# Kernel optimization log

Hardware: AMD Instinct MI355X
Metric: run time of the kernel (lower is better)

## Reference

```python
import jax, jax.numpy as jnp
import numpy as np
import math

D = 256        # embedding_size
NHEAD = 4
HD = D // NHEAD
FF = 2048      # torch TransformerEncoderLayer default dim_feedforward
NLAYER = 3
VOCAB = 30000
OLD = 2048     # resnet50 fc in_features
BPTT = 20
EOS = 2
PAD = 0
MAXLEN = 5000


def make_pe():
    position = np.arange(MAXLEN)[:, None].astype(np.float32)
    div_term = np.exp(np.arange(0, D, 2).astype(np.float32) * (-math.log(10000.0) / D))
    pe = np.zeros((MAXLEN, D), dtype=np.float32)
    pe[:, 0::2] = np.sin(position * div_term)
    pe[:, 1::2] = np.cos(position * div_term)
    return jnp.asarray(pe)  # [maxlen, d]

PE = make_pe()


def setup_inputs() -> dict:
    key = jax.random.key(0)
    ks = jax.random.split(key, 20)
    s = 0.02
    inp = {
        'image_feats': jax.random.normal(ks[0], (64, OLD), jnp.float32),
        'target_ingrs': jax.random.randint(ks[1], (64, BPTT), 0, VOCAB),
        'emb_table': jax.random.normal(ks[2], (VOCAB, D), jnp.float32) * s,
        'W_g2e': jax.random.normal(ks[3], (OLD, D), jnp.float32) * s,
        'b_g2e': jnp.zeros((D,), jnp.float32),
        'W_out': jax.random.normal(ks[4], (D, VOCAB), jnp.float32) * s,
        'b_out': jnp.zeros((VOCAB,), jnp.float32),
    }
    # per-layer transformer params
    Wqkv, bqkv, Wo, bo, W1, b1, W2, b2, g1, be1, g2, be2 = ([] for _ in range(12))
    k = ks[5]
    for l in range(NLAYER):
        k, *sub = jax.random.split(k, 7)
        Wqkv.append(jax.random.normal(sub[0], (D, 3 * D), jnp.float32) * s)
        bqkv.append(jnp.zeros((3 * D,), jnp.float32))
        Wo.append(jax.random.normal(sub[1], (D, D), jnp.float32) * s)
        bo.append(jnp.zeros((D,), jnp.float32))
        W1.append(jax.random.normal(sub[2], (D, FF), jnp.float32) * s)
        b1.append(jnp.zeros((FF,), jnp.float32))
        W2.append(jax.random.normal(sub[3], (FF, D), jnp.float32) * s)
        b2.append(jnp.zeros((D,), jnp.float32))
        g1.append(jnp.ones((D,), jnp.float32)); be1.append(jnp.zeros((D,), jnp.float32))
        g2.append(jnp.ones((D,), jnp.float32)); be2.append(jnp.zeros((D,), jnp.float32))
    stk = lambda xs: jnp.stack(xs)
    inp.update(Wqkv=stk(Wqkv), bqkv=stk(bqkv), Wo=stk(Wo), bo=stk(bo),
               W1=stk(W1), b1=stk(b1), W2=stk(W2), b2=stk(b2),
               g1=stk(g1), be1=stk(be1), g2=stk(g2), be2=stk(be2))
    return inp


def layernorm(x, g, b):
    mu = jnp.mean(x, -1, keepdims=True)
    var = jnp.var(x, -1, keepdims=True)
    return (x - mu) * jax.lax.rsqrt(var + 1e-5) * g + b


def encoder(x, params):
    # x: [S, B, D] (seq-first like torch). Post-norm encoder, ReLU FFN, no mask.
    (Wqkv, bqkv, Wo, bo, W1, b1, W2, b2, g1, be1, g2, be2) = params
    S, B, _ = x.shape
    for l in range(NLAYER):
        qkv = x @ Wqkv[l] + bqkv[l]                  # [S,B,3D]
        q, k, v = jnp.split(qkv, 3, axis=-1)
        def heads(t):  # [S,B,D] -> [B,H,S,hd]
            return t.reshape(S, B, NHEAD, HD).transpose(1, 2, 0, 3)
        q, k, v = heads(q), heads(k), heads(v)
        att = jnp.einsum('bhqd,bhkd->bhqk', q, k) / math.sqrt(HD)
        att = jax.nn.softmax(att, axis=-1)
        o = jnp.einsum('bhqk,bhkd->bhqd', att, v)    # [B,H,S,hd]
        o = o.transpose(2, 0, 1, 3).reshape(S, B, D)
        x = layernorm(x + o @ Wo[l] + bo[l], g1[l], be1[l])
        ff = jax.nn.relu(x @ W1[l] + b1[l]) @ W2[l] + b2[l]
        x = layernorm(x + ff, g2[l], be2[l])
    return x


def mask_from_eos_after(ids):
    # mult_before=False: mask[:,idx] = all(ids[:,1:idx+1] != EOS); mask[:,0]=1
    ne = (ids != EOS)
    ne = ne.at[:, 0].set(True)
    return jnp.cumprod(ne.astype(jnp.int32), axis=1)  # [B,S]


def reference(image_feats, target_ingrs, emb_table, W_g2e, b_g2e, W_out, b_out,
              Wqkv, bqkv, Wo, bo, W1, b1, W2, b2, g1, be1, g2, be2):
    params = (Wqkv, bqkv, Wo, bo, W1, b1, W2, b2, g1, be1, g2, be2)
    B = image_feats.shape[0]
    img_embed = image_feats @ W_g2e + b_g2e          # [B,D]
    bptt = target_ingrs.shape[1]

    # embeds buffer: [bptt, B, D]; position 0 = image embed (note: original code
    # never applies pos_encoder in predict(), so neither do we)
    embeds = jnp.zeros((bptt, B, D), jnp.float32).at[0].set(img_embed)

    probs_steps = []
    words_steps = []
    # loop over decode steps (fixed-length Python loop; each step re-encodes prefix,
    # faithful to original no-KV-cache behavior)
    for i in range(bptt):
        seq = embeds[: i + 1]                        # [i+1, B, D]
        out = encoder(seq, params)[-1]               # [B, D]
        logits = out @ W_out + b_out                 # [B, V]
        sm = jax.nn.softmax(logits, axis=-1)
        widx = jnp.argmax(sm, axis=-1)               # [B]
        probs_steps.append(sm)
        words_steps.append(widx)
        if i + 1 < bptt:
            embeds = embeds.at[i + 1].set(emb_table[widx])

    decoder_out = jnp.stack(probs_steps, axis=1)     # [B, bptt, V]
    sampled_word = jnp.stack(words_steps, axis=1)    # [B, bptt]
    eos = decoder_out[:, :, EOS]
    mask = mask_from_eos_after(target_ingrs)         # [B, bptt] int
    ingr_probs = jnp.max(decoder_out * mask[:, :, None].astype(jnp.float32), axis=1)
    sampled_word = jnp.where(mask == 0, PAD, sampled_word)
    return ingr_probs, sampled_word, eos
```

## Files before the change

### kernel.cpp

```cpp
#include <hip/hip_runtime.h>
#include <math.h>

#define D 256
#define NH 4
#define HDIM 64
#define FFD 2048
#define NL 3
#define VOC 30000
#define BPTT 20
#define BATCH 64
#define NMAX (BPTT*BATCH)

__global__ void k_mask(const int* __restrict__ ids, int* __restrict__ mask) {
  int b = threadIdx.x;
  int run = 1;
  for (int j = 0; j < BPTT; ++j) {
    if (j > 0 && ids[b*BPTT + j] == 2) run = 0;
    mask[b*BPTT + j] = run;
  }
}

__global__ __launch_bounds__(256) void k_img(const float* __restrict__ feats,
                                             const float* __restrict__ Wg,
                                             const float* __restrict__ bg,
                                             float* __restrict__ embeds) {
  __shared__ float xs[2048];
  int b = blockIdx.x, tid = threadIdx.x;
  for (int j = 0; j < 8; ++j) xs[tid + j*256] = feats[b*2048 + tid + j*256];
  __syncthreads();
  float acc = 0.f;
  for (int k = 0; k < 2048; k += 4) {
    float4 xv = *(const float4*)&xs[k];
    acc += xv.x * Wg[(k+0)*D + tid];
    acc += xv.y * Wg[(k+1)*D + tid];
    acc += xv.z * Wg[(k+2)*D + tid];
    acc += xv.w * Wg[(k+3)*D + tid];
  }
  embeds[b*D + tid] = acc + bg[tid];
}

__global__ __launch_bounds__(256) void k_gemm8(
    const float* __restrict__ A, int lda,
    const float* __restrict__ W,
    const float* __restrict__ bias,
    float* __restrict__ C, long pstride,
    int klen, int M, int relu)
{
  __shared__ float As[8][256];
  const int tid  = threadIdx.x;
  const int tok0 = blockIdx.x * 8;
  const int colb = blockIdx.y * 256;
  const int z    = blockIdx.z;
  const int kbeg = z * klen;
  C += (long)z * pstride;
  const int colg = tid & 63;
  const int tokg = tid >> 6;
  const int col  = colb + colg*4;
  int colL = col;
  if (colL > M-4) colL = M-4;

  float acc[2][4] = {{0.f,0.f,0.f,0.f},{0.f,0.f,0.f,0.f}};

  for (int k0 = 0; k0 < klen; k0 += 256) {
    __syncthreads();
#pragma unroll
    for (int j = 0; j < 8; ++j)
      As[j][tid] = A[(long)(tok0 + j)*lda + kbeg + k0 + tid];
    __syncthreads();
    const float* Wp = W + (long)(kbeg + k0)*M + colL;
#pragma unroll 2
    for (int kk = 0; kk < 256; kk += 4) {
      float a[2][4], w[4][4];
      *(float4*)a[0] = *(const float4*)&As[tokg*2+0][kk];
      *(float4*)a[1] = *(const float4*)&As[tokg*2+1][kk];
      *(float4*)w[0] = *(const float4*)(Wp + (long)(kk+0)*M);
      *(float4*)w[1] = *(const float4*)(Wp + (long)(kk+1)*M);
      *(float4*)w[2] = *(const float4*)(Wp + (long)(kk+2)*M);
      *(float4*)w[3] = *(const float4*)(Wp + (long)(kk+3)*M);
#pragma unroll
      for (int j = 0; j < 2; ++j)
#pragma unroll
        for (int c = 0; c < 4; ++c)
#pragma unroll
          for (int q = 0; q < 4; ++q)
            acc[j][c] += a[j][q] * w[q][c];
    }
  }

  if (col < M) {
    float bv[4] = {0.f,0.f,0.f,0.f};
    if (bias) *(float4*)bv = *(const float4*)(bias + col);
#pragma unroll
    for (int j = 0; j < 2; ++j) {
      float v[4];
#pragma unroll
      for (int c = 0; c < 4; ++c) {
        v[c] = acc[j][c] + bv[c];
        if (relu) v[c] = fmaxf(v[c], 0.f);
      }
      *(float4*)(C + (long)(tok0 + tokg*2 + j)*M + col) = *(float4*)v;
    }
  }
}

__global__ __launch_bounds__(256) void k_resln(
    const float* __restrict__ x, const float* __restrict__ parts, int nparts, long pstride,
    const float* __restrict__ bias, const float* __restrict__ g, const float* __restrict__ be,
    float* __restrict__ out)
{
  __shared__ float red[4];
  int tok = blockIdx.x, tid = threadIdx.x;
  float v = x[(long)tok*D + tid] + bias[tid];
  for (int p = 0; p < nparts; ++p) v += parts[(long)p*pstride + (long)tok*D + tid];

  float s = v;
  for (int off = 32; off; off >>= 1) s += __shfl_down(s, off);
  if ((tid & 63) == 0) red[tid >> 6] = s;
  __syncthreads();
  float mu = (red[0]+red[1]+red[2]+red[3]) * (1.0f/D);
  __syncthreads();
  float dv = v - mu;
  float q = dv*dv;
  for (int off = 32; off; off >>= 1) q += __shfl_down(q, off);
  if ((tid & 63) == 0) red[tid >> 6] = q;
  __syncthreads();
  float var = (red[0]+red[1]+red[2]+red[3]) * (1.0f/D);
  float inv = 1.0f / sqrtf(var + 1e-5f);
  out[(long)tok*D + tid] = dv * inv * g[tid] + be[tid];
}

__global__ __launch_bounds__(64) void k_attn(const float* __restrict__ qkv,
                                             float* __restrict__ o, int S)
{
  __shared__ float qs[BPTT*HDIM], ks[BPTT*HDIM], vs[BPTT*HDIM], ps[BPTT*(BPTT+1)];
  int bh = blockIdx.x;
  int b = bh & 63, h = bh >> 6;
  int d = threadIdx.x;
  for (int s = 0; s < S; ++s) {
    long base = (long)(s*BATCH + b)*(3*D) + h*HDIM + d;
    qs[s*HDIM+d] = qkv[base];
    ks[s*HDIM+d] = qkv[base + D];
    vs[s*HDIM+d] = qkv[base + 2*D];
  }
  __syncthreads();
  for (int p = d; p < S*S; p += 64) {
    int si = p / S, ti = p - si*S;
    float acc = 0.f;
#pragma unroll 4
    for (int k = 0; k < HDIM; ++k) acc += qs[si*HDIM+k] * ks[ti*HDIM+k];
    ps[si*(BPTT+1)+ti] = acc * 0.125f;
  }
  __syncthreads();
  if (d < S) {
    float m = -1e30f;
    for (int t = 0; t < S; ++t) m = fmaxf(m, ps[d*(BPTT+1)+t]);
    float sum = 0.f;
    for (int t = 0; t < S; ++t) { float e = expf(ps[d*(BPTT+1)+t] - m); ps[d*(BPTT+1)+t] = e; sum += e; }
    float inv = 1.0f / sum;
    for (int t = 0; t < S; ++t) ps[d*(BPTT+1)+t] *= inv;
  }
  __syncthreads();
  for (int s = 0; s < S; ++s) {
    float acc = 0.f;
    for (int t = 0; t < S; ++t) acc += ps[s*(BPTT+1)+t] * vs[t*HDIM+d];
    o[(long)(s*BATCH+b)*D + h*HDIM + d] = acc;
  }
}

__global__ __launch_bounds__(256) void k_vocab(
    const float* __restrict__ logits, const int* __restrict__ mask,
    float* __restrict__ out_probs, float* __restrict__ out_words, float* __restrict__ out_eos,
    const float* __restrict__ emb, float* __restrict__ embeds, int step)
{
  __shared__ float redA[4];
  __shared__ float r_s[4];
  __shared__ float r_em[4];
  __shared__ int   r_ei[4];
  int b = blockIdx.x, tid = threadIdx.x;
  const float* lrow = logits + (long)b*VOC;

  float m = -1e30f;
  for (int c = tid; c < VOC; c += 256) m = fmaxf(m, lrow[c]);
  for (int off = 32; off; off >>= 1) m = fmaxf(m, __shfl_down(m, off));
  if ((tid & 63) == 0) redA[tid >> 6] = m;
  __syncthreads();
  float gmax = fmaxf(fmaxf(redA[0],redA[1]), fmaxf(redA[2],redA[3]));
  __syncthreads();

  float s = 0.f, em = -1.0f;
  int ei = VOC;
  for (int c = tid; c < VOC; c += 256) {
    float e = expf(lrow[c] - gmax);
    s += e;
    if (e > em) { em = e; ei = c; }
  }
  for (int off = 32; off; off >>= 1) {
    float em2 = __shfl_down(em, off);
    int   ei2 = __shfl_down(ei, off);
    if (em2 > em || (em2 == em && ei2 < ei)) { em = em2; ei = ei2; }
    s += __shfl_down(s, off);
  }
  if ((tid & 63) == 0) { r_s[tid>>6] = s; r_em[tid>>6] = em; r_ei[tid>>6] = ei; }
  __syncthreads();
  float Ssum = r_s[0]+r_s[1]+r_s[2]+r_s[3];
  em = r_em[0]; ei = r_ei[0];
  for (int w = 1; w < 4; ++w)
    if (r_em[w] > em || (r_em[w] == em && r_ei[w] < ei)) { em = r_em[w]; ei = r_ei[w]; }

  int mk = mask[b*BPTT + step];

  for (int c = tid; c < VOC; c += 256) {
    float p = expf(lrow[c] - gmax) / Ssum;
    float* op = out_probs + (long)b*VOC + c;
    if (step == 0) *op = p;
    else if (mk)   *op = fmaxf(*op, p);
    if (c == 2) out_eos[b*BPTT + step] = p;
  }
  if (tid == 0) out_words[b*BPTT + step] = mk ? (float)ei : 0.0f;
  if (step + 1 < BPTT)
    embeds[(long)((step+1)*BATCH + b)*D + tid] = emb[(long)ei*D + tid];
}

extern "C" void kernel_launch(void* const* d_in, const int* in_sizes, int n_in,
                              void* d_out, int out_size, void* d_ws, size_t ws_size,
                              hipStream_t stream) {
  const float* image_feats = (const float*)d_in[0];
  const int*   target      = (const int*)  d_in[1];
  const float* emb_table   = (const float*)d_in[2];
  const float* W_g2e       = (const float*)d_in[3];
  const float* b_g2e       = (const float*)d_in[4];
  const float* W_out       = (const float*)d_in[5];
  const float* b_out       = (const float*)d_in[6];
  const float* Wqkv        = (const float*)d_in[7];
  const float* bqkv        = (const float*)d_in[8];
  const float* Wo          = (const float*)d_in[9];
  const float* bo          = (const float*)d_in[10];
  const float* W1          = (const float*)d_in[11];
  const float* b1          = (const float*)d_in[12];
  const float* W2          = (const float*)d_in[13];
  const float* b2          = (const float*)d_in[14];
  const float* g1          = (const float*)d_in[15];
  const float* be1         = (const float*)d_in[16];
  const float* g2          = (const float*)d_in[17];
  const float* be2         = (const float*)d_in[18];

  float* out_probs = (float*)d_out;
  float* out_words = out_probs + (long)BATCH*VOC;
  float* out_eos   = out_words + BATCH*BPTT;

  char* ws = (char*)d_ws;
  float* embeds = (float*)ws;  ws += sizeof(float)*(long)NMAX*D;
  float* xbuf   = (float*)ws;  ws += sizeof(float)*(long)NMAX*D;
  float* qkvb   = (float*)ws;  ws += sizeof(float)*(long)NMAX*3*D;
  float* obuf   = (float*)ws;  ws += sizeof(float)*(long)NMAX*D;
  float* pbuf   = (float*)ws;  ws += sizeof(float)*(long)4*NMAX*D;
  float* ffb    = (float*)ws;  ws += sizeof(float)*(long)NMAX*FFD;
  float* logits = (float*)ws;  ws += sizeof(float)*(long)BATCH*VOC;
  int*   maskb  = (int*)ws;    ws += sizeof(int)*BATCH*BPTT;

  k_mask<<<1, 64, 0, stream>>>(target, maskb);
  k_img<<<64, 256, 0, stream>>>(image_feats, W_g2e, b_g2e, embeds);

  for (int i = 0; i < BPTT; ++i) {
    int N = (i+1)*BATCH;
    for (int l = 0; l < NL; ++l) {
      const float* X = (l == 0) ? embeds : xbuf;
      k_gemm8<<<dim3(N/8, 3, 1), 256, 0, stream>>>(X, D, Wqkv + (long)l*D*3*D, bqkv + (long)l*3*D,
                                                   qkvb, 0, D, 3*D, 0);
      k_attn<<<dim3(BATCH*NH), 64, 0, stream>>>(qkvb, obuf, i+1);
      k_gemm8<<<dim3(N/8, 1, 1), 256, 0, stream>>>(obuf, D, Wo + (long)l*D*D, nullptr,
                                                   pbuf, 0, D, D, 0);
      k_resln<<<dim3(N), 256, 0, stream>>>(X, pbuf, 1, 0, bo + (long)l*D, g1 + (long)l*D, be1 + (long)l*D, xbuf);
      k_gemm8<<<dim3(N/8, FFD/256, 1), 256, 0, stream>>>(xbuf, D, W1 + (long)l*D*FFD, b1 + (long)l*FFD,
                                                         ffb, 0, D, FFD, 1);
      k_gemm8<<<dim3(N/8, 1, 4), 256, 0, stream>>>(ffb, FFD, W2 + (long)l*FFD*D, nullptr,
                                                   pbuf, (long)NMAX*D, FFD/4, D, 0);
      k_resln<<<dim3(N), 256, 0, stream>>>(xbuf, pbuf, 4, (long)NMAX*D, b2 + (long)l*D, g2 + (long)l*D, be2 + (long)l*D, xbuf);
    }
    k_gemm8<<<dim3(BATCH/8, (VOC+255)/256, 1), 256, 0, stream>>>(xbuf + (long)i*BATCH*D, D, W_out, b_out,
                                                                 logits, 0, D, VOC, 0);
    k_vocab<<<dim3(BATCH), 256, 0, stream>>>(logits, maskb, out_probs, out_words, out_eos,
                                             emb_table, embeds, i);
  }
}
```

Baseline: 10.87 ms.

## Replace per-op kernel launches with a single cooperative persistent megakernel

Fuses all stages of the decode loop into one cooperative kernel that uses grid-wide syncs between phases, so the roughly 700 separate launches disappear. It also fuses the Wo GEMM with the first residual+LayerNorm, fuses the FF1 GEMM with ReLU and a partial FF2 GEMM so the FF activation buffer is never written out, and gives attention four wavefronts per block. The cost is grid.sync overhead at each phase, a grid size hardcoded to 256 CUs, and load imbalance on the small early steps.

```diff
diff --git a/kernel.cpp b/kernel.cpp
--- a/kernel.cpp
+++ b/kernel.cpp
@@ -1,5 +1,8 @@
 #include <hip/hip_runtime.h>
+#include <hip/hip_cooperative_groups.h>
 #include <math.h>
+
+namespace cg = cooperative_groups;
 
 #define D 256
 #define NH 4
@@ -11,275 +14,380 @@
 #define BATCH 64
 #define NMAX (BPTT*BATCH)
 
-__global__ void k_mask(const int* __restrict__ ids, int* __restrict__ mask) {
-  int b = threadIdx.x;
-  int run = 1;
-  for (int j = 0; j < BPTT; ++j) {
-    if (j > 0 && ids[b*BPTT + j] == 2) run = 0;
-    mask[b*BPTT + j] = run;
+struct Params {
+  const float* image_feats;
+  const int*   target;
+  const float* emb_table;
+  const float* W_g2e;
+  const float* b_g2e;
+  const float* W_out;
+  const float* b_out;
+  const float* Wqkv; const float* bqkv;
+  const float* Wo;   const float* bo;
+  const float* W1;   const float* b1;
+  const float* W2;   const float* b2;
+  const float* g1;   const float* be1;
+  const float* g2;   const float* be2;
+  float* out_probs; float* out_words; float* out_eos;
+  float* embeds; float* xbuf; float* qkvb; float* obuf; float* pbuf; float* logits;
+  int* maskb;
+};
+
+union Smem {
+  struct { float As[8][256]; float ffs[8][256]; } g;
+  struct { float qs[BPTT*HDIM], ks[BPTT*HDIM], vs[BPTT*HDIM],
+                 ps[BPTT*(BPTT+1)]; } a;
+  struct { float red[4]; float r_s[4]; float r_em[4]; int r_ei[4]; } v;
+  float xs[2048];
+};
+
+__device__ __forceinline__ void tile_acc(const float (*As)[256], const float* __restrict__ Wp,
+                                         int M, int tokg, float acc[2][4]) {
+#pragma unroll 2
+  for (int kk = 0; kk < 256; kk += 4) {
+    float a0[4], a1[4], w[4][4];
+    *(float4*)a0 = *(const float4*)&As[tokg*2+0][kk];
+    *(float4*)a1 = *(const float4*)&As[tokg*2+1][kk];
+#pragma unroll
+    for (int q = 0; q < 4; ++q)
+      *(float4*)w[q] = *(const float4*)(Wp + (long)(kk+q)*M);
+#pragma unroll
+    for (int c = 0; c < 4; ++c)
+#pragma unroll
+      for (int q = 0; q < 4; ++q) {
+        acc[0][c] += a0[q]*w[q][c];
+        acc[1][c] += a1[q]*w[q][c];
+      }
   }
 }
 
-__global__ __launch_bounds__(256) void k_img(const float* __restrict__ feats,
-                                             const float* __restrict__ Wg,
-                                             const float* __restrict__ bg,
-                                             float* __restrict__ embeds) {
-  __shared__ float xs[2048];
-  int b = blockIdx.x, tid = threadIdx.x;
-  for (int j = 0; j < 8; ++j) xs[tid + j*256] = feats[b*2048 + tid + j*256];
-  __syncthreads();
-  float acc = 0.f;
-  for (int k = 0; k < 2048; k += 4) {
-    float4 xv = *(const float4*)&xs[k];
-    acc += xv.x * Wg[(k+0)*D + tid];
-    acc += xv.y * Wg[(k+1)*D + tid];
-    acc += xv.z * Wg[(k+2)*D + tid];
-    acc += xv.w * Wg[(k+3)*D + tid];
-  }
-  embeds[b*D + tid] = acc + bg[tid];
-}
-
-__global__ __launch_bounds__(256) void k_gemm8(
-    const float* __restrict__ A, int lda,
-    const float* __restrict__ W,
-    const float* __restrict__ bias,
-    float* __restrict__ C, long pstride,
-    int klen, int M, int relu)
-{
-  __shared__ float As[8][256];
-  const int tid  = threadIdx.x;
-  const int tok0 = blockIdx.x * 8;
-  const int colb = blockIdx.y * 256;
-  const int z    = blockIdx.z;
-  const int kbeg = z * klen;
-  C += (long)z * pstride;
-  const int colg = tid & 63;
-  const int tokg = tid >> 6;
-  const int col  = colb + colg*4;
-  int colL = col;
-  if (colL > M-4) colL = M-4;
-
-  float acc[2][4] = {{0.f,0.f,0.f,0.f},{0.f,0.f,0.f,0.f}};
-
-  for (int k0 = 0; k0 < klen; k0 += 256) {
+__global__ __launch_bounds__(256, 4) void mega(Params p) {
+  cg::grid_group grid = cg::this_grid();
+  const int wgid = blockIdx.x, nwg = gridDim.x, tid = threadIdx.x;
+  const int colg = tid & 63, tokg = tid >> 6;
+  __shared__ Smem sm;
+
+  if (wgid == 0 && tid < BATCH) {
+    int run = 1;
+    for (int j = 0; j < BPTT; ++j) {
+      if (j > 0 && p.target[tid*BPTT + j] == 2) run = 0;
+      p.maskb[tid*BPTT + j] = run;
+    }
+  }
+  for (int b = wgid; b < BATCH; b += nwg) {
     __syncthreads();
-#pragma unroll
-    for (int j = 0; j < 8; ++j)
-      As[j][tid] = A[(long)(tok0 + j)*lda + kbeg + k0 + tid];
+    for (int j = 0; j < 8; ++j) sm.xs[tid + j*256] = p.image_feats[b*2048 + tid + j*256];
     __syncthreads();
-    const float* Wp = W + (long)(kbeg + k0)*M + colL;
-#pragma unroll 2
-    for (int kk = 0; kk < 256; kk += 4) {
-      float a[2][4], w[4][4];
-      *(float4*)a[0] = *(const float4*)&As[tokg*2+0][kk];
-      *(float4*)a[1] = *(const float4*)&As[tokg*2+1][kk];
-      *(float4*)w[0] = *(const float4*)(Wp + (long)(kk+0)*M);
-      *(float4*)w[1] = *(const float4*)(Wp + (long)(kk+1)*M);
-      *(float4*)w[2] = *(const float4*)(Wp + (long)(kk+2)*M);
-      *(float4*)w[3] = *(const float4*)(Wp + (long)(kk+3)*M);
-#pragma unroll
-      for (int j = 0; j < 2; ++j)
-#pragma unroll
-        for (int c = 0; c < 4; ++c)
-#pragma unroll
-          for (int q = 0; q < 4; ++q)
-            acc[j][c] += a[j][q] * w[q][c];
-    }
-  }
-
-  if (col < M) {
-    float bv[4] = {0.f,0.f,0.f,0.f};
-    if (bias) *(float4*)bv = *(const float4*)(bias + col);
-#pragma unroll
-    for (int j = 0; j < 2; ++j) {
-      float v[4];
-#pragma unroll
-      for (int c = 0; c < 4; ++c) {
-        v[c] = acc[j][c] + bv[c];
-        if (relu) v[c] = fmaxf(v[c], 0.f);
-      }
-      *(float4*)(C + (long)(tok0 + tokg*2 + j)*M + col) = *(float4*)v;
-    }
-  }
-}
-
-__global__ __launch_bounds__(256) void k_resln(
-    const float* __restrict__ x, const float* __restrict__ parts, int nparts, long pstride,
-    const float* __restrict__ bias, const float* __restrict__ g, const float* __restrict__ be,
-    float* __restrict__ out)
-{
-  __shared__ float red[4];
-  int tok = blockIdx.x, tid = threadIdx.x;
-  float v = x[(long)tok*D + tid] + bias[tid];
-  for (int p = 0; p < nparts; ++p) v += parts[(long)p*pstride + (long)tok*D + tid];
-
-  float s = v;
-  for (int off = 32; off; off >>= 1) s += __shfl_down(s, off);
-  if ((tid & 63) == 0) red[tid >> 6] = s;
-  __syncthreads();
-  float mu = (red[0]+red[1]+red[2]+red[3]) * (1.0f/D);
-  __syncthreads();
-  float dv = v - mu;
-  float q = dv*dv;
-  for (int off = 32; off; off >>= 1) q += __shfl_down(q, off);
-  if ((tid & 63) == 0) red[tid >> 6] = q;
-  __syncthreads();
-  float var = (red[0]+red[1]+red[2]+red[3]) * (1.0f/D);
-  float inv = 1.0f / sqrtf(var + 1e-5f);
-  out[(long)tok*D + tid] = dv * inv * g[tid] + be[tid];
-}
-
-__global__ __launch_bounds__(64) void k_attn(const float* __restrict__ qkv,
-                                             float* __restrict__ o, int S)
-{
-  __shared__ float qs[BPTT*HDIM], ks[BPTT*HDIM], vs[BPTT*HDIM], ps[BPTT*(BPTT+1)];
-  int bh = blockIdx.x;
-  int b = bh & 63, h = bh >> 6;
-  int d = threadIdx.x;
-  for (int s = 0; s < S; ++s) {
-    long base = (long)(s*BATCH + b)*(3*D) + h*HDIM + d;
-    qs[s*HDIM+d] = qkv[base];
-    ks[s*HDIM+d] = qkv[base + D];
-    vs[s*HDIM+d] = qkv[base + 2*D];
-  }
-  __syncthreads();
-  for (int p = d; p < S*S; p += 64) {
-    int si = p / S, ti = p - si*S;
     float acc = 0.f;
+    for (int k = 0; k < 2048; k += 4) {
+      float4 xv = *(const float4*)&sm.xs[k];
+      acc += xv.x * p.W_g2e[(k+0)*D + tid];
+      acc += xv.y * p.W_g2e[(k+1)*D + tid];
+      acc += xv.z * p.W_g2e[(k+2)*D + tid];
+      acc += xv.w * p.W_g2e[(k+3)*D + tid];
+    }
+    p.embeds[b*D + tid] = acc + p.b_g2e[tid];
+  }
+  grid.sync();
+
+  for (int i = 0; i < BPTT; ++i) {
+    const int S = i + 1, N = S * BATCH, ntok8 = N >> 3;
+
+    for (int l = 0; l < NL; ++l) {
+      const float* X = (l == 0) ? p.embeds : p.xbuf;
+
+      {
+        const float* Wl = p.Wqkv + (long)l*D*3*D;
+        const float* bl = p.bqkv + l*3*D;
+        const int ntiles = ntok8 * 3;
+        for (int t = wgid; t < ntiles; t += nwg) {
+          const int tx = t % ntok8, ty = t / ntok8;
+          const int tok0 = tx*8, col = ty*256 + colg*4;
+          __syncthreads();
+#pragma unroll
+          for (int j = 0; j < 8; ++j) sm.g.As[j][tid] = X[(long)(tok0+j)*D + tid];
+          __syncthreads();
+          float acc[2][4] = {{0,0,0,0},{0,0,0,0}};
+          tile_acc(sm.g.As, Wl + col, 3*D, tokg, acc);
+          float bv[4]; *(float4*)bv = *(const float4*)(bl + col);
+#pragma unroll
+          for (int j = 0; j < 2; ++j) {
+            float v[4];
+#pragma unroll
+            for (int c = 0; c < 4; ++c) v[c] = acc[j][c] + bv[c];
+            *(float4*)(p.qkvb + (long)(tok0+tokg*2+j)*3*D + col) = *(float4*)v;
+          }
+        }
+      }
+      grid.sync();
+
+      {
+        const int d = tid & 63, g4 = tid >> 6;
+        for (int bh = wgid; bh < BATCH*NH; bh += nwg) {
+          const int b = bh & 63, h = bh >> 6;
+          __syncthreads();
+          for (int s = g4; s < S; s += 4) {
+            long base = (long)(s*BATCH + b)*(3*D) + h*HDIM + d;
+            sm.a.qs[s*HDIM+d] = p.qkvb[base];
+            sm.a.ks[s*HDIM+d] = p.qkvb[base + D];
+            sm.a.vs[s*HDIM+d] = p.qkvb[base + 2*D];
+          }
+          __syncthreads();
+          for (int q = tid; q < S*S; q += 256) {
+            int si = q / S, ti = q - si*S;
+            float acc = 0.f;
 #pragma unroll 4
-    for (int k = 0; k < HDIM; ++k) acc += qs[si*HDIM+k] * ks[ti*HDIM+k];
-    ps[si*(BPTT+1)+ti] = acc * 0.125f;
-  }
-  __syncthreads();
-  if (d < S) {
-    float m = -1e30f;
-    for (int t = 0; t < S; ++t) m = fmaxf(m, ps[d*(BPTT+1)+t]);
-    float sum = 0.f;
-    for (int t = 0; t < S; ++t) { float e = expf(ps[d*(BPTT+1)+t] - m); ps[d*(BPTT+1)+t] = e; sum += e; }
-    float inv = 1.0f / sum;
-    for (int t = 0; t < S; ++t) ps[d*(BPTT+1)+t] *= inv;
-  }
-  __syncthreads();
-  for (int s = 0; s < S; ++s) {
-    float acc = 0.f;
-    for (int t = 0; t < S; ++t) acc += ps[s*(BPTT+1)+t] * vs[t*HDIM+d];
-    o[(long)(s*BATCH+b)*D + h*HDIM + d] = acc;
-  }
-}
-
-__global__ __launch_bounds__(256) void k_vocab(
-    const float* __restrict__ logits, const int* __restrict__ mask,
-    float* __restrict__ out_probs, float* __restrict__ out_words, float* __restrict__ out_eos,
-    const float* __restrict__ emb, float* __restrict__ embeds, int step)
-{
-  __shared__ float redA[4];
-  __shared__ float r_s[4];
-  __shared__ float r_em[4];
-  __shared__ int   r_ei[4];
-  int b = blockIdx.x, tid = threadIdx.x;
-  const float* lrow = logits + (long)b*VOC;
-
-  float m = -1e30f;
-  for (int c = tid; c < VOC; c += 256) m = fmaxf(m, lrow[c]);
-  for (int off = 32; off; off >>= 1) m = fmaxf(m, __shfl_down(m, off));
-  if ((tid & 63) == 0) redA[tid >> 6] = m;
-  __syncthreads();
-  float gmax = fmaxf(fmaxf(redA[0],redA[1]), fmaxf(redA[2],redA[3]));
-  __syncthreads();
-
-  float s = 0.f, em = -1.0f;
-  int ei = VOC;
-  for (int c = tid; c < VOC; c += 256) {
-    float e = expf(lrow[c] - gmax);
-    s += e;
-    if (e > em) { em = e; ei = c; }
-  }
-  for (int off = 32; off; off >>= 1) {
-    float em2 = __shfl_down(em, off);
-    int   ei2 = __shfl_down(ei, off);
-    if (em2 > em || (em2 == em && ei2 < ei)) { em = em2; ei = ei2; }
-    s += __shfl_down(s, off);
-  }
-  if ((tid & 63) == 0) { r_s[tid>>6] = s; r_em[tid>>6] = em; r_ei[tid>>6] = ei; }
-  __syncthreads();
-  float Ssum = r_s[0]+r_s[1]+r_s[2]+r_s[3];
-  em = r_em[0]; ei = r_ei[0];
-  for (int w = 1; w < 4; ++w)
-    if (r_em[w] > em || (r_em[w] == em && r_ei[w] < ei)) { em = r_em[w]; ei = r_ei[w]; }
-
-  int mk = mask[b*BPTT + step];
-
-  for (int c = tid; c < VOC; c += 256) {
-    float p = expf(lrow[c] - gmax) / Ssum;
-    float* op = out_probs + (long)b*VOC + c;
-    if (step == 0) *op = p;
-    else if (mk)   *op = fmaxf(*op, p);
-    if (c == 2) out_eos[b*BPTT + step] = p;
-  }
-  if (tid == 0) out_words[b*BPTT + step] = mk ? (float)ei : 0.0f;
-  if (step + 1 < BPTT)
-    embeds[(long)((step+1)*BATCH + b)*D + tid] = emb[(long)ei*D + tid];
+            for (int k = 0; k < HDIM; ++k) acc += sm.a.qs[si*HDIM+k] * sm.a.ks[ti*HDIM+k];
+            sm.a.ps[si*(BPTT+1)+ti] = acc * 0.125f;
+          }
+          __syncthreads();
+          if (tid < S) {
+            float m = -1e30f;
+            for (int t2 = 0; t2 < S; ++t2) m = fmaxf(m, sm.a.ps[tid*(BPTT+1)+t2]);
+            float sum = 0.f;
+            for (int t2 = 0; t2 < S; ++t2) {
+              float e = expf(sm.a.ps[tid*(BPTT+1)+t2] - m);
+              sm.a.ps[tid*(BPTT+1)+t2] = e; sum += e;
+            }
+            float inv = 1.0f/sum;
+            for (int t2 = 0; t2 < S; ++t2) sm.a.ps[tid*(BPTT+1)+t2] *= inv;
+          }
+          __syncthreads();
+          for (int s = g4; s < S; s += 4) {
+            float acc = 0.f;
+            for (int t2 = 0; t2 < S; ++t2) acc += sm.a.ps[s*(BPTT+1)+t2] * sm.a.vs[t2*HDIM+d];
+            p.obuf[(long)(s*BATCH+b)*D + h*HDIM + d] = acc;
+          }
+        }
+      }
+      grid.sync();
+
+      {
+        const float* Wl  = p.Wo  + (long)l*D*D;
+        const float* bol = p.bo  + l*D;
+        const float* g1l = p.g1  + l*D;
+        const float* be1l= p.be1 + l*D;
+        const int col = colg*4;
+        for (int t = wgid; t < ntok8; t += nwg) {
+          const int tok0 = t*8;
+          __syncthreads();
+#pragma unroll
+          for (int j = 0; j < 8; ++j) sm.g.As[j][tid] = p.obuf[(long)(tok0+j)*D + tid];
+          __syncthreads();
+          float acc[2][4] = {{0,0,0,0},{0,0,0,0}};
+          tile_acc(sm.g.As, Wl + col, D, tokg, acc);
+#pragma unroll
+          for (int j = 0; j < 2; ++j) {
+            const int tok = tok0 + tokg*2 + j;
+            float v[4];
+#pragma unroll
+            for (int c = 0; c < 4; ++c) v[c] = acc[j][c] + X[(long)tok*D + col + c] + bol[col + c];
+            float s = v[0]+v[1]+v[2]+v[3];
+            for (int off = 32; off; off >>= 1) s += __shfl_down(s, off);
+            float mu = __shfl(s, 0) * (1.0f/D);
+            float q = 0.f;
+#pragma unroll
+            for (int c = 0; c < 4; ++c) { float dv = v[c]-mu; q += dv*dv; }
+            for (int off = 32; off; off >>= 1) q += __shfl_down(q, off);
+            float var = __shfl(q, 0) * (1.0f/D);
+            float inv = 1.0f/sqrtf(var + 1e-5f);
+#pragma unroll
+            for (int c = 0; c < 4; ++c)
+              p.xbuf[(long)tok*D + col + c] = (v[c]-mu)*inv*g1l[col+c] + be1l[col+c];
+          }
+        }
+      }
+      grid.sync();
+
+      {
+        const float* W1l = p.W1 + (long)l*D*FFD;
+        const float* b1l = p.b1 + l*FFD;
+        const float* W2l = p.W2 + (long)l*FFD*D;
+        const int col = colg*4;
+        const int ntiles = ntok8*8;
+        for (int t = wgid; t < ntiles; t += nwg) {
+          const int tx = t % ntok8, ty = t / ntok8;
+          const int tok0 = tx*8, fc0 = ty*256;
+          __syncthreads();
+#pragma unroll
+          for (int j = 0; j < 8; ++j) sm.g.As[j][tid] = p.xbuf[(long)(tok0+j)*D + tid];
+          __syncthreads();
+          float acc[2][4] = {{0,0,0,0},{0,0,0,0}};
+          tile_acc(sm.g.As, W1l + fc0 + col, FFD, tokg, acc);
+#pragma unroll
+          for (int j = 0; j < 2; ++j)
+#pragma unroll
+            for (int c = 0; c < 4; ++c)
+              sm.g.ffs[tokg*2+j][col+c] = fmaxf(acc[j][c] + b1l[fc0+col+c], 0.f);
+          __syncthreads();
+          float acc2[2][4] = {{0,0,0,0},{0,0,0,0}};
+          tile_acc(sm.g.ffs, W2l + (long)fc0*D + col, D, tokg, acc2);
+#pragma unroll
+          for (int j = 0; j < 2; ++j)
+            *(float4*)(p.pbuf + ((long)ty*NMAX + tok0+tokg*2+j)*D + col) = *(float4*)acc2[j];
+        }
+      }
+      grid.sync();
+
+      {
+        const float* b2l = p.b2 + l*D;
+        const float* g2l = p.g2 + l*D;
+        const float* be2l= p.be2 + l*D;
+        const int c0 = colg*4;
+        for (int tk = wgid*4 + tokg; tk < N; tk += nwg*4) {
+          float v[4];
+          *(float4*)v = *(const float4*)(p.xbuf + (long)tk*D + c0);
+          float4 bb = *(const float4*)(b2l + c0);
+          v[0]+=bb.x; v[1]+=bb.y; v[2]+=bb.z; v[3]+=bb.w;
+#pragma unroll
+          for (int q = 0; q < 8; ++q) {
+            float4 pp = *(const float4*)(p.pbuf + ((long)q*NMAX + tk)*D + c0);
+            v[0]+=pp.x; v[1]+=pp.y; v[2]+=pp.z; v[3]+=pp.w;
+          }
+          float s = v[0]+v[1]+v[2]+v[3];
+          for (int off = 32; off; off >>= 1) s += __shfl_down(s, off);
+          float mu = __shfl(s, 0) * (1.0f/D);
+          float q2 = 0.f;
+#pragma unroll
+          for (int c = 0; c < 4; ++c) { float dv = v[c]-mu; q2 += dv*dv; }
+          for (int off = 32; off; off >>= 1) q2 += __shfl_down(q2, off);
+          float var = __shfl(q2, 0) * (1.0f/D);
+          float inv = 1.0f/sqrtf(var + 1e-5f);
+          float4 gg = *(const float4*)(g2l + c0);
+          float4 ee = *(const float4*)(be2l + c0);
+          float o[4];
+          o[0]=(v[0]-mu)*inv*gg.x+ee.x; o[1]=(v[1]-mu)*inv*gg.y+ee.y;
+          o[2]=(v[2]-mu)*inv*gg.z+ee.z; o[3]=(v[3]-mu)*inv*gg.w+ee.w;
+          *(float4*)(p.xbuf + (long)tk*D + c0) = *(float4*)o;
+        }
+      }
+      grid.sync();
+    }
+
+    {
+      const float* A = p.xbuf + (long)i*BATCH*D;
+      const int ntiles = 8 * ((VOC + 255) >> 8);
+      for (int t = wgid; t < ntiles; t += nwg) {
+        const int tx = t & 7, ty = t >> 3;
+        const int tok0 = tx*8;
+        const int col = ty*256 + colg*4;
+        const int colL = col > VOC-4 ? VOC-4 : col;
+        __syncthreads();
+#pragma unroll
+        for (int j = 0; j < 8; ++j) sm.g.As[j][tid] = A[(long)(tok0+j)*D + tid];
+        __syncthreads();
+        float acc[2][4] = {{0,0,0,0},{0,0,0,0}};
+        tile_acc(sm.g.As, p.W_out + colL, VOC, tokg, acc);
+        if (col < VOC) {
+          float bv[4]; *(float4*)bv = *(const float4*)(p.b_out + col);
+#pragma unroll
+          for (int j = 0; j < 2; ++j) {
+            float v[4];
+#pragma unroll
+            for (int c = 0; c < 4; ++c) v[c] = acc[j][c] + bv[c];
+            *(float4*)(p.logits + (long)(tok0+tokg*2+j)*VOC + col) = *(float4*)v;
+          }
+        }
+      }
+    }
+    grid.sync();
+
+    {
+      for (int b = wgid; b < BATCH; b += nwg) {
+        const float* lrow = p.logits + (long)b*VOC;
+        __syncthreads();
+        float m = -1e30f;
+        for (int c = tid; c < VOC; c += 256) m = fmaxf(m, lrow[c]);
+        for (int off = 32; off; off >>= 1) m = fmaxf(m, __shfl_down(m, off));
+        if (colg == 0) sm.v.red[tokg] = m;
+        __syncthreads();
+        float gmax = fmaxf(fmaxf(sm.v.red[0],sm.v.red[1]), fmaxf(sm.v.red[2],sm.v.red[3]));
+        __syncthreads();
+        float s = 0.f, em = -1.0f; int ei = VOC;
+        for (int c = tid; c < VOC; c += 256) {
+          float e = expf(lrow[c] - gmax);
+          s += e;
+          if (e > em) { em = e; ei = c; }
+        }
+        for (int off = 32; off; off >>= 1) {
+          float em2 = __shfl_down(em, off);
+          int   ei2 = __shfl_down(ei, off);
+          if (em2 > em || (em2 == em && ei2 < ei)) { em = em2; ei = ei2; }
+          s += __shfl_down(s, off);
+        }
+        if (colg == 0) { sm.v.r_s[tokg] = s; sm.v.r_em[tokg] = em; sm.v.r_ei[tokg] = ei; }
+        __syncthreads();
+        float Ssum = sm.v.r_s[0]+sm.v.r_s[1]+sm.v.r_s[2]+sm.v.r_s[3];
+        em = sm.v.r_em[0]; ei = sm.v.r_ei[0];
+        for (int w = 1; w < 4; ++w)
+          if (sm.v.r_em[w] > em || (sm.v.r_em[w] == em && sm.v.r_ei[w] < ei)) { em = sm.v.r_em[w]; ei = sm.v.r_ei[w]; }
+        const int mk = p.maskb[b*BPTT + i];
+        for (int c = tid; c < VOC; c += 256) {
+          float prob = expf(lrow[c] - gmax) / Ssum;
+          float* op = p.out_probs + (long)b*VOC + c;
+          if (i == 0) *op = prob;
+          else if (mk) *op = fmaxf(*op, prob);
+          if (c == 2) p.out_eos[b*BPTT + i] = prob;
+        }
+        if (tid == 0) p.out_words[b*BPTT + i] = mk ? (float)ei : 0.0f;
+        if (i + 1 < BPTT)
+          p.embeds[(long)((i+1)*BATCH + b)*D + tid] = p.emb_table[(long)ei*D + tid];
+      }
+    }
+    grid.sync();
+  }
 }
 
 extern "C" void kernel_launch(void* const* d_in, const int* in_sizes, int n_in,
                               void* d_out, int out_size, void* d_ws, size_t ws_size,
                               hipStream_t stream) {
-  const float* image_feats = (const float*)d_in[0];
-  const int*   target      = (const int*)  d_in[1];
-  const float* emb_table   = (const float*)d_in[2];
-  const float* W_g2e       = (const float*)d_in[3];
-  const float* b_g2e       = (const float*)d_in[4];
-  const float* W_out       = (const float*)d_in[5];
-  const float* b_out       = (const float*)d_in[6];
-  const float* Wqkv        = (const float*)d_in[7];
-  const float* bqkv        = (const float*)d_in[8];
-  const float* Wo          = (const float*)d_in[9];
-  const float* bo          = (const float*)d_in[10];
-  const float* W1          = (const float*)d_in[11];
-  const float* b1          = (const float*)d_in[12];
-  const float* W2          = (const float*)d_in[13];
-  const float* b2          = (const float*)d_in[14];
-  const float* g1          = (const float*)d_in[15];
-  const float* be1         = (const float*)d_in[16];
-  const float* g2          = (const float*)d_in[17];
-  const float* be2         = (const float*)d_in[18];
+  Params P;
+  P.image_feats = (const float*)d_in[0];
+  P.target      = (const int*)  d_in[1];
+  P.emb_table   = (const float*)d_in[2];
+  P.W_g2e       = (const float*)d_in[3];
+  P.b_g2e       = (const float*)d_in[4];
+  P.W_out       = (const float*)d_in[5];
+  P.b_out       = (const float*)d_in[6];
+  P.Wqkv        = (const float*)d_in[7];
+  P.bqkv        = (const float*)d_in[8];
+  P.Wo          = (const float*)d_in[9];
+  P.bo          = (const float*)d_in[10];
+  P.W1          = (const float*)d_in[11];
+  P.b1          = (const float*)d_in[12];
+  P.W2          = (const float*)d_in[13];
+  P.b2          = (const float*)d_in[14];
+  P.g1          = (const float*)d_in[15];
+  P.be1         = (const float*)d_in[16];
+  P.g2          = (const float*)d_in[17];
+  P.be2         = (const float*)d_in[18];
 
   float* out_probs = (float*)d_out;
-  float* out_words = out_probs + (long)BATCH*VOC;
-  float* out_eos   = out_words + BATCH*BPTT;
+  P.out_probs = out_probs;
+  P.out_words = out_probs + (long)BATCH*VOC;
+  P.out_eos   = P.out_words + BATCH*BPTT;
 
   char* ws = (char*)d_ws;
-  float* embeds = (float*)ws;  ws += sizeof(float)*(long)NMAX*D;
-  float* xbuf   = (float*)ws;  ws += sizeof(float)*(long)NMAX*D;
-  float* qkvb   = (float*)ws;  ws += sizeof(float)*(long)NMAX*3*D;
-  float* obuf   = (float*)ws;  ws += sizeof(float)*(long)NMAX*D;
-  float* pbuf   = (float*)ws;  ws += sizeof(float)*(long)4*NMAX*D;
-  float* ffb    = (float*)ws;  ws += sizeof(float)*(long)NMAX*FFD;
-  float* logits = (float*)ws;  ws += sizeof(float)*(long)BATCH*VOC;
-  int*   maskb  = (int*)ws;    ws += sizeof(int)*BATCH*BPTT;
-
-  k_mask<<<1, 64, 0, stream>>>(target, maskb);
-  k_img<<<64, 256, 0, stream>>>(image_feats, W_g2e, b_g2e, embeds);
-
-  for (int i = 0; i < BPTT; ++i) {
-    int N = (i+1)*BATCH;
-    for (int l = 0; l < NL; ++l) {
-      const float* X = (l == 0) ? embeds : xbuf;
-      k_gemm8<<<dim3(N/8, 3, 1), 256, 0, stream>>>(X, D, Wqkv + (long)l*D*3*D, bqkv + (long)l*3*D,
-                                                   qkvb, 0, D, 3*D, 0);
-      k_attn<<<dim3(BATCH*NH), 64, 0, stream>>>(qkvb, obuf, i+1);
-      k_gemm8<<<dim3(N/8, 1, 1), 256, 0, stream>>>(obuf, D, Wo + (long)l*D*D, nullptr,
-                                                   pbuf, 0, D, D, 0);
-      k_resln<<<dim3(N), 256, 0, stream>>>(X, pbuf, 1, 0, bo + (long)l*D, g1 + (long)l*D, be1 + (long)l*D, xbuf);
-      k_gemm8<<<dim3(N/8, FFD/256, 1), 256, 0, stream>>>(xbuf, D, W1 + (long)l*D*FFD, b1 + (long)l*FFD,
-                                                         ffb, 0, D, FFD, 1);
-      k_gemm8<<<dim3(N/8, 1, 4), 256, 0, stream>>>(ffb, FFD, W2 + (long)l*FFD*D, nullptr,
-                                                   pbuf, (long)NMAX*D, FFD/4, D, 0);
-      k_resln<<<dim3(N), 256, 0, stream>>>(xbuf, pbuf, 4, (long)NMAX*D, b2 + (long)l*D, g2 + (long)l*D, be2 + (long)l*D, xbuf);
-    }
-    k_gemm8<<<dim3(BATCH/8, (VOC+255)/256, 1), 256, 0, stream>>>(xbuf + (long)i*BATCH*D, D, W_out, b_out,
-                                                                 logits, 0, D, VOC, 0);
-    k_vocab<<<dim3(BATCH), 256, 0, stream>>>(logits, maskb, out_probs, out_words, out_eos,
-                                             emb_table, embeds, i);
+  P.embeds = (float*)ws;  ws += sizeof(float)*(long)NMAX*D;
+  P.xbuf   = (float*)ws;  ws += sizeof(float)*(long)NMAX*D;
+  P.qkvb   = (float*)ws;  ws += sizeof(float)*(long)NMAX*3*D;
+  P.obuf   = (float*)ws;  ws += sizeof(float)*(long)NMAX*D;
+  P.pbuf   = (float*)ws;  ws += sizeof(float)*(long)8*NMAX*D;
+  P.logits = (float*)ws;  ws += sizeof(float)*(long)BATCH*VOC;
+  P.maskb  = (int*)ws;    ws += sizeof(int)*BATCH*BPTT;
+
+  static int nwg = 0;
+  if (nwg == 0) {
+    int maxb = 0;
+    hipOccupancyMaxActiveBlocksPerMultiprocessor(&maxb, mega, 256, 0);
+    if (maxb < 1) maxb = 1;
+    if (maxb > 4) maxb = 4;
+    nwg = maxb * 256;
+  }
+  void* args[] = { &P };
+  hipError_t err = hipLaunchCooperativeKernel((void*)mega, dim3(nwg), dim3(256), args, 0, stream);
+  if (err != hipSuccess && nwg > 256) {
+    nwg = 256;
+    hipLaunchCooperativeKernel((void*)mega, dim3(nwg), dim3(256), args, 0, stream);
   }
 }
```

Result: slower. 29.22 ms (+168.8%).
